# Kernel optimization log

Measured on AMD Instinct MI355X. Metric: run time of the kernel, lower is better.

Reference implementation:

```python
import jax, jax.numpy as jnp
import numpy as np
from functools import partial

PERPLEXITY = 30.0
TOL = 1e-05
K = int(3 * PERPLEXITY)  # neighbors kept after dropping self
N_CAT = 8
N_TRIES = 50


def setup_inputs() -> dict:
    key = jax.random.key(0)
    k1, k2 = jax.random.split(key)
    x = jax.random.normal(k1, (8192, 64), dtype=jnp.float32)
    batch_id = jax.random.randint(k2, (8192,), 0, N_CAT, dtype=jnp.int32)
    return {"x": x, "batch_id": batch_id}


def _knn(x):
    # squared Euclidean pairwise distances [N, N]
    sq = jnp.sum(x * x, axis=-1)
    d2 = sq[:, None] + sq[None, :] - 2.0 * (x @ x.T)
    d2 = jnp.maximum(d2, 0.0)
    neg, idx = jax.lax.top_k(-d2, K + 1)  # nearest K+1 incl. self
    dist = jnp.sqrt(jnp.maximum(-neg[:, 1:], 0.0))  # drop self -> [N, K] Euclidean
    return dist, idx[:, 1:]


def _hbeta(dist, beta):
    # dist: [N, K], beta: [N] -> entropy H [N], normalized P [N, K]
    P = jnp.exp(-dist * beta[:, None])
    Psum = jnp.sum(P, axis=1)
    safe = Psum > 0
    Psafe = jnp.where(safe, Psum, 1.0)
    H = jnp.where(safe, jnp.log(Psafe) + beta * jnp.sum(dist * P, axis=1) / Psafe, 0.0)
    Pn = jnp.where(safe[:, None], P / Psafe[:, None], 0.0)
    return H, Pn


def _beta_search(dist):
    N = dist.shape[0]
    logU = jnp.log(jnp.float32(PERPLEXITY))
    beta = jnp.ones((N,), dist.dtype)
    bmin = jnp.full((N,), -jnp.inf, dist.dtype)
    bmax = jnp.full((N,), jnp.inf, dist.dtype)
    H, P = _hbeta(dist, beta)
    Hdiff = H - logU

    def step(carry, _):
        beta, bmin, bmax, H, P, Hdiff = carry
        done = jnp.abs(Hdiff) < TOL
        pos = Hdiff > 0
        nbmin = jnp.where(pos, beta, bmin)
        nbmax = jnp.where(pos, bmax, beta)
        b_up = jnp.where(jnp.isfinite(bmax), (beta + bmax) * 0.5, beta * 2.0)
        b_dn = jnp.where(jnp.isfinite(bmin), (beta + bmin) * 0.5, beta * 0.5)
        nbeta = jnp.where(pos, b_up, b_dn)
        beta2 = jnp.where(done, beta, nbeta)
        bmin2 = jnp.where(done, bmin, nbmin)
        bmax2 = jnp.where(done, bmax, nbmax)
        Hn, Pn = _hbeta(dist, beta2)
        H2 = jnp.where(done, H, Hn)
        P2 = jnp.where(done[:, None], P, Pn)
        return (beta2, bmin2, bmax2, H2, P2, H2 - logU), None

    (beta, bmin, bmax, H, P, Hdiff), _ = jax.lax.scan(
        step, (beta, bmin, bmax, H, P, Hdiff), None, length=N_TRIES)
    return H, P


@jax.jit
def reference(x, batch_id):
    dist, idx = _knn(x)                      # [N, K], [N, K]
    H, P = _beta_search(dist)                # [N], [N, K]
    nbr_labels = batch_id[idx]               # [N, K]
    onehot = (nbr_labels[:, :, None] == jnp.arange(N_CAT)[None, None, :]).astype(P.dtype)
    contrib = jnp.einsum('nk,nkc->nc', P, onehot)   # per-category prob mass
    simpson = jnp.sum(contrib * contrib, axis=-1) + jnp.where(H == 0, -1.0, 0.0)
    return 1.0 / simpson
```

## Files before the change

### kernel.cpp

```cpp
#include <hip/hip_runtime.h>
#include <math.h>
#include <float.h>

#define N 8192
#define D 64
#define NK 90
#define NK1 (NK + 1)
#define BMR 32
#define NBAND (N / BMR)
#define HCOL (N / 2)
#define NWAVE 16
#define BCOL (NWAVE * 32)
#define NSTEP (HCOL / BCOL)
#define NBIN 256
#define CAP 192
#define SQS 6

typedef __attribute__((ext_vector_type(8))) short short8v;
typedef __attribute__((ext_vector_type(16))) float f32x16;

__device__ __forceinline__ unsigned short f2bf(float f) {
    unsigned u = __float_as_uint(f);
    unsigned r = (u + 0x7FFFu + ((u >> 16) & 1u)) >> 16;
    return (unsigned short)r;
}
__device__ __forceinline__ float bf2f(unsigned short h) {
    return __uint_as_float(((unsigned)h) << 16);
}

__global__ void k_prep(const float* __restrict__ x, unsigned short* __restrict__ xhi,
                       unsigned short* __restrict__ xlo, float* __restrict__ sq,
                       int* __restrict__ maxbits) {
    const int r = blockIdx.x * 256 + threadIdx.x;
    const float4* p = (const float4*)(x + (size_t)r * D);
    ushort4* ph = (ushort4*)(xhi + (size_t)r * D);
    ushort4* pl = (ushort4*)(xlo + (size_t)r * D);
    float s = 0.f;
#pragma unroll
    for (int q = 0; q < D / 4; ++q) {
        float4 v = p[q];
        s += v.x * v.x + v.y * v.y + v.z * v.z + v.w * v.w;
        ushort4 hh, ll;
        hh.x = f2bf(v.x); ll.x = f2bf(v.x - bf2f(hh.x));
        hh.y = f2bf(v.y); ll.y = f2bf(v.y - bf2f(hh.y));
        hh.z = f2bf(v.z); ll.z = f2bf(v.z - bf2f(hh.z));
        hh.w = f2bf(v.w); ll.w = f2bf(v.w - bf2f(hh.w));
        ph[q] = hh; pl[q] = ll;
    }
    sq[r] = s;
    float m = s;
    for (int o = 32; o > 0; o >>= 1) m = fmaxf(m, __shfl_xor(m, o, 64));
    if ((threadIdx.x & 63) == 0) atomicMax(maxbits, __float_as_int(m));
}

__device__ __forceinline__ f32x16 dot_acc(const unsigned short* __restrict__ xhi,
                                          const unsigned short* __restrict__ xlo,
                                          const short8v* ahi, const short8v* alo,
                                          int gj, int h) {
    f32x16 acc;
#pragma unroll
    for (int i = 0; i < 16; ++i) acc[i] = 0.f;
    const unsigned short* bh = xhi + (size_t)gj * D + 8 * h;
    const unsigned short* bl = xlo + (size_t)gj * D + 8 * h;
#pragma unroll
    for (int ks = 0; ks < 4; ++ks) {
        short8v bhiv = *(const short8v*)(bh + ks * 16);
        short8v blov = *(const short8v*)(bl + ks * 16);
        acc = __builtin_amdgcn_mfma_f32_32x32x16_bf16(ahi[ks], bhiv, acc, 0, 0, 0);
        acc = __builtin_amdgcn_mfma_f32_32x32x16_bf16(ahi[ks], blov, acc, 0, 0, 0);
        acc = __builtin_amdgcn_mfma_f32_32x32x16_bf16(alo[ks], bhiv, acc, 0, 0, 0);
    }
    return acc;
}

__global__ __launch_bounds__(1024) void k_knn2(const unsigned short* __restrict__ xhi,
                                               const unsigned short* __restrict__ xlo,
                                               const float* __restrict__ sq,
                                               const int* __restrict__ maxbits,
                                               float* __restrict__ gbufv,
                                               unsigned short* __restrict__ gbufi,
                                               int* __restrict__ gcnt) {
    __shared__ int hist[BMR][NBIN];
    __shared__ float bufv[BMR][CAP];
    __shared__ unsigned short bufi[BMR][CAP];
    __shared__ int cnt[BMR];
    __shared__ float bsf[BMR];

    const int tid = threadIdx.x;
    const int lane = tid & 63;
    const int h = lane >> 5;
    const int wv = tid >> 6;
    const int band = blockIdx.x >> 1;
    const int half = blockIdx.x & 1;
    const int colbase = half * HCOL;
    const int row0 = band * BMR;

    for (int e = tid; e < BMR * NBIN; e += 1024) ((int*)hist)[e] = 0;
    if (tid < BMR) cnt[tid] = 0;

    const float hi = 4.0f * __int_as_float(maxbits[0]) + 1.0f;
    const float scale = (float)NBIN / hi;
    const float inv_scale = hi / (float)NBIN;
    const float ns = -2.0f * scale;

    short8v ahi_[4], alo_[4];
    const size_t abase = (size_t)(row0 + (lane & 31)) * D + 8 * h;
#pragma unroll
    for (int ks = 0; ks < 4; ++ks) {
        ahi_[ks] = *(const short8v*)(xhi + abase + ks * 16);
        alo_[ks] = *(const short8v*)(xlo + abase + ks * 16);
    }
    float sia_s[4][4];
#pragma unroll
    for (int q = 0; q < 4; ++q) {
        float4 t = *(const float4*)(sq + row0 + 8 * q + 4 * h);
        sia_s[q][0] = t.x * scale; sia_s[q][1] = t.y * scale;
        sia_s[q][2] = t.z * scale; sia_s[q][3] = t.w * scale;
    }
    __syncthreads();

    for (int s = 0; s < NSTEP; ++s) {
        const int gj = colbase + s * BCOL + wv * 32 + (lane & 31);
        const float sjs = sq[gj] * scale;
        f32x16 acc = dot_acc(xhi, xlo, ahi_, alo_, gj, h);
#pragma unroll
        for (int q = 0; q < 4; ++q)
#pragma unroll
            for (int j = 0; j < 4; ++j) {
                const float binf = fmaf(ns, acc[4 * q + j], sia_s[q][j] + sjs);
                const int bin = (int)fminf(fmaxf(binf, 0.f), (float)(NBIN - 1));
                atomicAdd(&hist[8 * q + 4 * h + j][bin], 1);
            }
    }
    __syncthreads();

#pragma unroll 1
    for (int rr = 0; rr < 2; ++rr) {
        const int r = wv * 2 + rr;
        int pc[4]; int ssum = 0;
#pragma unroll
        for (int b = 0; b < 4; ++b) { pc[b] = hist[r][lane * 4 + b]; ssum += pc[b]; }
        int incl = ssum;
        for (int o = 1; o < 64; o <<= 1) {
            int t = __shfl_up(incl, o, 64);
            if (lane >= o) incl += t;
        }
        const int excl = incl - ssum;
        const bool has = (excl < NK1) && (incl >= NK1);
        const unsigned long long m = __ballot(has);
        const int src = __ffsll((unsigned long long)m) - 1;
        int bsel = NBIN - 1;
        if (has) {
            int c = excl;
#pragma unroll
            for (int b = 0; b < 4; ++b) {
                c += pc[b];
                if (c >= NK1) { bsel = lane * 4 + b; break; }
            }
        }
        bsel = __shfl(bsel, src, 64);
        if (lane == 0) bsf[r] = (float)(bsel + 1);
    }
    __syncthreads();

    float bsr[4][4];
#pragma unroll
    for (int q = 0; q < 4; ++q) {
        float4 t = *(const float4*)(&bsf[8 * q + 4 * h]);
        bsr[q][0] = t.x; bsr[q][1] = t.y; bsr[q][2] = t.z; bsr[q][3] = t.w;
    }

    for (int s = 0; s < NSTEP; ++s) {
        const int gj = colbase + s * BCOL + wv * 32 + (lane & 31);
        const float sjs = sq[gj] * scale;
        f32x16 acc = dot_acc(xhi, xlo, ahi_, alo_, gj, h);
#pragma unroll
        for (int q = 0; q < 4; ++q)
#pragma unroll
            for (int j = 0; j < 4; ++j) {
                const int rl = 8 * q + 4 * h + j;
                const float binf = fmaf(ns, acc[4 * q + j], sia_s[q][j] + sjs);
                const bool pred = binf < bsr[q][j];
                const unsigned long long mm = __ballot(pred);
                if (mm) {
                    const unsigned mh = (unsigned)(mm >> (h * 32));
                    int base = 0;
                    if ((lane & 31) == 0) base = atomicAdd(&cnt[rl], __popc(mh));
                    base = __shfl(base, 0, 32);
                    if (pred) {
                        const int pos = base + __popc(mh & ((1u << (lane & 31)) - 1u));
                        if (pos < CAP) {
                            bufv[rl][pos] = binf * inv_scale;
                            bufi[rl][pos] = (unsigned short)gj;
                        }
                    }
                }
            }
    }
    __syncthreads();

    for (int e = tid; e < BMR * CAP; e += 1024) {
        const int r = e / CAP, k = e - r * CAP;
        const size_t dst = ((size_t)(row0 + r) * 2 + half) * CAP + k;
        gbufv[dst] = bufv[r][k];
        gbufi[dst] = bufi[r][k];
    }
    if (tid < BMR) {
        int n = cnt[tid];
        gcnt[(row0 + tid) * 2 + half] = n < CAP ? n : CAP;
    }
}

__global__ __launch_bounds__(1024) void k_sel_lisi(const float* __restrict__ gbufv,
                                                   const unsigned short* __restrict__ gbufi,
                                                   const int* __restrict__ gcnt,
                                                   const int* __restrict__ batch,
                                                   float* __restrict__ out) {
    __shared__ float scrv[NWAVE][96];
    __shared__ unsigned short scri[NWAVE][96];

    const int lane = threadIdx.x & 63;
    const int w = threadIdx.x >> 6;
    const int row = blockIdx.x * NWAVE + w;
    const unsigned long long lt = (1ull << lane) - 1ull;

    const int n0 = gcnt[row * 2 + 0];
    const int n1 = gcnt[row * 2 + 1];
    const float* bv = gbufv + (size_t)row * 2 * CAP;
    const unsigned short* bi = gbufi + (size_t)row * 2 * CAP;

    float fv[SQS]; unsigned short fi[SQS]; unsigned uv[SQS]; bool va[SQS];
#pragma unroll
    for (int q = 0; q < SQS; ++q) {
        const int e = lane + 64 * q;
        const int hh = e >= CAP;
        const int k = e - hh * CAP;
        const bool inb = k < (hh ? n1 : n0);
        fv[q] = inb ? bv[e] : 0.f;
        fi[q] = inb ? bi[e] : (unsigned short)0;
        va[q] = inb && (fi[q] != (unsigned short)row);
        uv[q] = __float_as_uint(fv[q]);
    }
    unsigned Tlo = 0u, Thi = 0x7F800000u;
    while (Thi - Tlo > 1u) {
        unsigned Tm = Tlo + ((Thi - Tlo) >> 1);
        int c = 0;
#pragma unroll
        for (int q = 0; q < SQS; ++q)
            c += __popcll(__ballot(va[q] && uv[q] <= Tm));
        if (c >= NK) Thi = Tm; else Tlo = Tm;
    }
    int base = 0;
#pragma unroll
    for (int q = 0; q < SQS; ++q) {
        bool p = va[q] && uv[q] < Thi;
        unsigned long long m = __ballot(p);
        if (p) { int pos = base + __popcll(m & lt); scrv[w][pos] = fv[q]; scri[w][pos] = fi[q]; }
        base += __popcll(m);
    }
    const int c1 = base;
    const int room = NK - c1;
    int tb = 0;
#pragma unroll
    for (int q = 0; q < SQS; ++q) {
        bool p = va[q] && uv[q] == Thi;
        unsigned long long m = __ballot(p);
        if (p) {
            int o = tb + __popcll(m & lt);
            if (o < room) { scrv[w][c1 + o] = fv[q]; scri[w][c1 + o] = fi[q]; }
        }
        tb += __popcll(m);
    }

    const float logU = 3.4011974f;
    const float d0 = sqrtf(fmaxf(scrv[w][lane], 0.f));
    const int i0 = scri[w][lane];
    const bool v1 = lane < (NK - 64);
    const float d1 = v1 ? sqrtf(fmaxf(scrv[w][64 + lane], 0.f)) : 0.f;
    const int i1 = v1 ? scri[w][64 + lane] : 0;
    const int l0 = batch[i0];
    const int l1 = v1 ? batch[i1] : -1;

    float beta = 1.f, bmin = -INFINITY, bmax = INFINITY;
    float P0, P1, S, H;

    auto hbeta = [&](float b) {
        P0 = __expf(-d0 * b);
        P1 = v1 ? __expf(-d1 * b) : 0.f;
        float s = P0 + P1;
        float ww = d0 * P0 + (v1 ? d1 * P1 : 0.f);
        for (int o = 32; o > 0; o >>= 1) {
            s += __shfl_xor(s, o, 64);
            ww += __shfl_xor(ww, o, 64);
        }
        S = s;
        H = (S > 0.f) ? (__logf(S) + b * ww / S) : 0.f;
    };

    hbeta(beta);
    float Hdiff = H - logU;
    for (int it = 0; it < 50; ++it) {
        if (fabsf(Hdiff) < 1e-5f) break;
        if (Hdiff > 0.f) {
            bmin = beta;
            beta = isinf(bmax) ? beta * 2.f : 0.5f * (beta + bmax);
        } else {
            bmax = beta;
            beta = isinf(bmin) ? beta * 0.5f : 0.5f * (beta + bmin);
        }
        hbeta(beta);
        Hdiff = H - logU;
    }

    const float Pn0 = (S > 0.f) ? P0 / S : 0.f;
    const float Pn1 = (S > 0.f && v1) ? P1 / S : 0.f;

    float simpson = 0.f;
#pragma unroll
    for (int c = 0; c < 8; ++c) {
        float v = (l0 == c ? Pn0 : 0.f) + (l1 == c ? Pn1 : 0.f);
        for (int o = 32; o > 0; o >>= 1) v += __shfl_xor(v, o, 64);
        simpson += v * v;
    }
    if (H == 0.f) simpson -= 1.f;
    if (lane == 0) out[row] = 1.f / simpson;
}

extern "C" void kernel_launch(void* const* d_in, const int* in_sizes, int n_in,
                              void* d_out, int out_size, void* d_ws, size_t ws_size,
                              hipStream_t stream) {
    const float* x = (const float*)d_in[0];
    const int* batch = (const int*)d_in[1];
    float* out = (float*)d_out;

    float* sq = (float*)d_ws;
    int* maxbits = (int*)(sq + N);
    int* gcnt = maxbits + 4;
    unsigned short* xhi = (unsigned short*)(gcnt + 2 * N);
    unsigned short* xlo = xhi + (size_t)N * D;
    float* gbufv = (float*)(xlo + (size_t)N * D);
    unsigned short* gbufi = (unsigned short*)(gbufv + (size_t)N * 2 * CAP);

    k_prep<<<N / 256, 256, 0, stream>>>(x, xhi, xlo, sq, maxbits);
    k_knn2<<<2 * NBAND, 1024, 0, stream>>>(xhi, xlo, sq, maxbits, gbufv, gbufi, gcnt);
    k_sel_lisi<<<N / NWAVE, 1024, 0, stream>>>(gbufv, gbufi, gcnt, batch, out);
}
```

Measured before the change: 236.6 us.

## Process two column tiles per wave in kNN passes and split prep rows across lanes

```diff
diff --git a/kernel.cpp b/kernel.cpp
--- a/kernel.cpp
+++ b/kernel.cpp
@@ -10,8 +10,7 @@
 #define NBAND (N / BMR)
 #define HCOL (N / 2)
 #define NWAVE 16
-#define BCOL (NWAVE * 32)
-#define NSTEP (HCOL / BCOL)
+#define NIT 4
 #define NBIN 256
 #define CAP 192
 #define SQS 6
@@ -31,13 +30,14 @@
 __global__ void k_prep(const float* __restrict__ x, unsigned short* __restrict__ xhi,
                        unsigned short* __restrict__ xlo, float* __restrict__ sq,
                        int* __restrict__ maxbits) {
-    const int r = blockIdx.x * 256 + threadIdx.x;
-    const float4* p = (const float4*)(x + (size_t)r * D);
-    ushort4* ph = (ushort4*)(xhi + (size_t)r * D);
-    ushort4* pl = (ushort4*)(xlo + (size_t)r * D);
+    const int t = blockIdx.x * 256 + threadIdx.x;
+    const int r = t >> 2, part = t & 3;
+    const float4* p = (const float4*)(x + (size_t)r * D + part * 16);
+    ushort4* ph = (ushort4*)(xhi + (size_t)r * D + part * 16);
+    ushort4* pl = (ushort4*)(xlo + (size_t)r * D + part * 16);
     float s = 0.f;
 #pragma unroll
-    for (int q = 0; q < D / 4; ++q) {
+    for (int q = 0; q < 4; ++q) {
         float4 v = p[q];
         s += v.x * v.x + v.y * v.y + v.z * v.z + v.w * v.w;
         ushort4 hh, ll;
@@ -47,39 +47,47 @@
         hh.w = f2bf(v.w); ll.w = f2bf(v.w - bf2f(hh.w));
         ph[q] = hh; pl[q] = ll;
     }
-    sq[r] = s;
+    s += __shfl_xor(s, 1, 64);
+    s += __shfl_xor(s, 2, 64);
+    if (part == 0) sq[r] = s;
     float m = s;
-    for (int o = 32; o > 0; o >>= 1) m = fmaxf(m, __shfl_xor(m, o, 64));
+    for (int o = 4; o < 64; o <<= 1) m = fmaxf(m, __shfl_xor(m, o, 64));
     if ((threadIdx.x & 63) == 0) atomicMax(maxbits, __float_as_int(m));
 }
 
-__device__ __forceinline__ f32x16 dot_acc(const unsigned short* __restrict__ xhi,
-                                          const unsigned short* __restrict__ xlo,
-                                          const short8v* ahi, const short8v* alo,
-                                          int gj, int h) {
-    f32x16 acc;
-#pragma unroll
-    for (int i = 0; i < 16; ++i) acc[i] = 0.f;
-    const unsigned short* bh = xhi + (size_t)gj * D + 8 * h;
-    const unsigned short* bl = xlo + (size_t)gj * D + 8 * h;
+__device__ __forceinline__ void dot2(const unsigned short* __restrict__ xhi,
+                                     const unsigned short* __restrict__ xlo,
+                                     const short8v* ahi, const short8v* alo,
+                                     int gj0, int gj1, int h,
+                                     f32x16& acc0, f32x16& acc1) {
+#pragma unroll
+    for (int i = 0; i < 16; ++i) { acc0[i] = 0.f; acc1[i] = 0.f; }
+    const unsigned short* b0h = xhi + (size_t)gj0 * D + 8 * h;
+    const unsigned short* b0l = xlo + (size_t)gj0 * D + 8 * h;
+    const unsigned short* b1h = xhi + (size_t)gj1 * D + 8 * h;
+    const unsigned short* b1l = xlo + (size_t)gj1 * D + 8 * h;
 #pragma unroll
     for (int ks = 0; ks < 4; ++ks) {
-        short8v bhiv = *(const short8v*)(bh + ks * 16);
-        short8v blov = *(const short8v*)(bl + ks * 16);
-        acc = __builtin_amdgcn_mfma_f32_32x32x16_bf16(ahi[ks], bhiv, acc, 0, 0, 0);
-        acc = __builtin_amdgcn_mfma_f32_32x32x16_bf16(ahi[ks], blov, acc, 0, 0, 0);
-        acc = __builtin_amdgcn_mfma_f32_32x32x16_bf16(alo[ks], bhiv, acc, 0, 0, 0);
-    }
-    return acc;
-}
-
-__global__ __launch_bounds__(1024) void k_knn2(const unsigned short* __restrict__ xhi,
-                                               const unsigned short* __restrict__ xlo,
-                                               const float* __restrict__ sq,
-                                               const int* __restrict__ maxbits,
-                                               float* __restrict__ gbufv,
-                                               unsigned short* __restrict__ gbufi,
-                                               int* __restrict__ gcnt) {
+        short8v h0 = *(const short8v*)(b0h + ks * 16);
+        short8v l0 = *(const short8v*)(b0l + ks * 16);
+        short8v h1 = *(const short8v*)(b1h + ks * 16);
+        short8v l1 = *(const short8v*)(b1l + ks * 16);
+        acc0 = __builtin_amdgcn_mfma_f32_32x32x16_bf16(ahi[ks], h0, acc0, 0, 0, 0);
+        acc1 = __builtin_amdgcn_mfma_f32_32x32x16_bf16(ahi[ks], h1, acc1, 0, 0, 0);
+        acc0 = __builtin_amdgcn_mfma_f32_32x32x16_bf16(ahi[ks], l0, acc0, 0, 0, 0);
+        acc1 = __builtin_amdgcn_mfma_f32_32x32x16_bf16(ahi[ks], l1, acc1, 0, 0, 0);
+        acc0 = __builtin_amdgcn_mfma_f32_32x32x16_bf16(alo[ks], h0, acc0, 0, 0, 0);
+        acc1 = __builtin_amdgcn_mfma_f32_32x32x16_bf16(alo[ks], h1, acc1, 0, 0, 0);
+    }
+}
+
+__global__ __launch_bounds__(1024, 4) void k_knn2(const unsigned short* __restrict__ xhi,
+                                                  const unsigned short* __restrict__ xlo,
+                                                  const float* __restrict__ sq,
+                                                  const int* __restrict__ maxbits,
+                                                  float* __restrict__ gbufv,
+                                                  unsigned short* __restrict__ gbufi,
+                                                  int* __restrict__ gcnt) {
     __shared__ int hist[BMR][NBIN];
     __shared__ float bufv[BMR][CAP];
     __shared__ unsigned short bufi[BMR][CAP];
@@ -119,17 +127,24 @@
     }
     __syncthreads();
 
-    for (int s = 0; s < NSTEP; ++s) {
-        const int gj = colbase + s * BCOL + wv * 32 + (lane & 31);
-        const float sjs = sq[gj] * scale;
-        f32x16 acc = dot_acc(xhi, xlo, ahi_, alo_, gj, h);
+    for (int it = 0; it < NIT; ++it) {
+        const int gj0 = colbase + it * (NWAVE * 64) + wv * 64 + (lane & 31);
+        const int gj1 = gj0 + 32;
+        const float sjs0 = sq[gj0] * scale;
+        const float sjs1 = sq[gj1] * scale;
+        f32x16 a0, a1;
+        dot2(xhi, xlo, ahi_, alo_, gj0, gj1, h, a0, a1);
 #pragma unroll
         for (int q = 0; q < 4; ++q)
 #pragma unroll
             for (int j = 0; j < 4; ++j) {
-                const float binf = fmaf(ns, acc[4 * q + j], sia_s[q][j] + sjs);
-                const int bin = (int)fminf(fmaxf(binf, 0.f), (float)(NBIN - 1));
-                atomicAdd(&hist[8 * q + 4 * h + j][bin], 1);
+                const int rl = 8 * q + 4 * h + j;
+                const float b0 = fmaf(ns, a0[4 * q + j], sia_s[q][j] + sjs0);
+                const float b1 = fmaf(ns, a1[4 * q + j], sia_s[q][j] + sjs1);
+                const int i0 = (int)fminf(fmaxf(b0, 0.f), (float)(NBIN - 1));
+                const int i1 = (int)fminf(fmaxf(b1, 0.f), (float)(NBIN - 1));
+                atomicAdd(&hist[rl][i0], 1);
+                atomicAdd(&hist[rl][i1], 1);
             }
     }
     __syncthreads();
@@ -170,29 +185,32 @@
         bsr[q][0] = t.x; bsr[q][1] = t.y; bsr[q][2] = t.z; bsr[q][3] = t.w;
     }
 
-    for (int s = 0; s < NSTEP; ++s) {
-        const int gj = colbase + s * BCOL + wv * 32 + (lane & 31);
-        const float sjs = sq[gj] * scale;
-        f32x16 acc = dot_acc(xhi, xlo, ahi_, alo_, gj, h);
+    for (int it = 0; it < NIT; ++it) {
+        const int gj0 = colbase + it * (NWAVE * 64) + wv * 64 + (lane & 31);
+        const int gj1 = gj0 + 32;
+        const float sjs0 = sq[gj0] * scale;
+        const float sjs1 = sq[gj1] * scale;
+        f32x16 a0, a1;
+        dot2(xhi, xlo, ahi_, alo_, gj0, gj1, h, a0, a1);
 #pragma unroll
         for (int q = 0; q < 4; ++q)
 #pragma unroll
             for (int j = 0; j < 4; ++j) {
                 const int rl = 8 * q + 4 * h + j;
-                const float binf = fmaf(ns, acc[4 * q + j], sia_s[q][j] + sjs);
-                const bool pred = binf < bsr[q][j];
-                const unsigned long long mm = __ballot(pred);
-                if (mm) {
-                    const unsigned mh = (unsigned)(mm >> (h * 32));
-                    int base = 0;
-                    if ((lane & 31) == 0) base = atomicAdd(&cnt[rl], __popc(mh));
-                    base = __shfl(base, 0, 32);
-                    if (pred) {
-                        const int pos = base + __popc(mh & ((1u << (lane & 31)) - 1u));
-                        if (pos < CAP) {
-                            bufv[rl][pos] = binf * inv_scale;
-                            bufi[rl][pos] = (unsigned short)gj;
-                        }
+                const float b0 = fmaf(ns, a0[4 * q + j], sia_s[q][j] + sjs0);
+                const float b1 = fmaf(ns, a1[4 * q + j], sia_s[q][j] + sjs1);
+                if (b0 < bsr[q][j]) {
+                    const int pos = atomicAdd(&cnt[rl], 1);
+                    if (pos < CAP) {
+                        bufv[rl][pos] = b0 * inv_scale;
+                        bufi[rl][pos] = (unsigned short)gj0;
+                    }
+                }
+                if (b1 < bsr[q][j]) {
+                    const int pos = atomicAdd(&cnt[rl], 1);
+                    if (pos < CAP) {
+                        bufv[rl][pos] = b1 * inv_scale;
+                        bufi[rl][pos] = (unsigned short)gj1;
                     }
                 }
             }
@@ -341,7 +359,7 @@
     float* gbufv = (float*)(xlo + (size_t)N * D);
     unsigned short* gbufi = (unsigned short*)(gbufv + (size_t)N * 2 * CAP);
 
-    k_prep<<<N / 256, 256, 0, stream>>>(x, xhi, xlo, sq, maxbits);
+    k_prep<<<N * 4 / 256, 256, 0, stream>>>(x, xhi, xlo, sq, maxbits);
     k_knn2<<<2 * NBAND, 1024, 0, stream>>>(xhi, xlo, sq, maxbits, gbufv, gbufi, gcnt);
     k_sel_lisi<<<N / NWAVE, 1024, 0, stream>>>(gbufv, gbufi, gcnt, batch, out);
 }
```

Result: slower. 253.7 us (+7.2%).
